# Kernel optimization log

Measured on AMD Instinct MI355X. Metric: run time of the kernel, lower is better.

The kernel has to match this reference:

```python
import jax, jax.numpy as jnp
import numpy as np

D_MODEL = 768
NUM_HEADS = 12
HEAD_DIM = D_MODEL // NUM_HEADS  # 64, also rotary dim
INTERMEDIATE = 1152
WINDOW = 128          # config.local_attention (layer_id=1 -> local layer)
ROPE_BASE = 10000.0   # local_rope_theta
EPS = 1e-5


def layer_norm_nocenter(x, gamma):
    # keras LayerNormalization(center=False): mean-subtract, no beta
    mu = jnp.mean(x, axis=-1, keepdims=True)
    var = jnp.var(x, axis=-1, keepdims=True)
    return (x - mu) * jax.lax.rsqrt(var + EPS) * gamma


def rotate_half(x):
    x1, x2 = jnp.split(x, 2, axis=-1)
    return jnp.concatenate([-x2, x1], axis=-1)


def setup_inputs() -> dict:
    key = jax.random.key(0)
    ks = jax.random.split(key, 7)
    B, S = 4, 2048
    hidden_states = jax.random.normal(ks[0], (B, S, D_MODEL), dtype=jnp.float32)
    attention_mask = jnp.zeros((B, 1, S, S), dtype=jnp.float32)  # no padding
    s = 0.02
    attn_norm_gamma = jnp.ones((D_MODEL,), dtype=jnp.float32)
    wqkv = jax.random.normal(ks[1], (D_MODEL, 3 * D_MODEL), dtype=jnp.float32) * s
    wo_attn = jax.random.normal(ks[2], (D_MODEL, D_MODEL), dtype=jnp.float32) * s
    mlp_norm_gamma = jnp.ones((D_MODEL,), dtype=jnp.float32)
    wi = jax.random.normal(ks[3], (D_MODEL, 2 * INTERMEDIATE), dtype=jnp.float32) * s
    wo_mlp = jax.random.normal(ks[4], (INTERMEDIATE, D_MODEL), dtype=jnp.float32) * s
    return {
        'hidden_states': hidden_states,
        'attention_mask': attention_mask,
        'attn_norm_gamma': attn_norm_gamma,
        'wqkv': wqkv,
        'wo_attn': wo_attn,
        'mlp_norm_gamma': mlp_norm_gamma,
        'wi': wi,
        'wo_mlp': wo_mlp,
    }


def reference(hidden_states, attention_mask, attn_norm_gamma, wqkv, wo_attn,
              mlp_norm_gamma, wi, wo_mlp):
    B, S, Dm = hidden_states.shape
    H, Dh = NUM_HEADS, HEAD_DIM

    # RoPE cache (NTKScaling with scaling_factor=1 -> plain RoPE)
    idx = jnp.arange(0, Dh, 2, dtype=jnp.float32)
    inv_freq = 1.0 / (ROPE_BASE ** (idx / Dh))          # [Dh/2]
    t = jnp.arange(S, dtype=jnp.float32)
    freqs = t[:, None] * inv_freq[None, :]              # [S, Dh/2]
    emb = jnp.concatenate([freqs, freqs], axis=-1)      # [S, Dh]
    cos = jnp.cos(emb)[None, None]                      # [1,1,S,Dh]
    sin = jnp.sin(emb)[None, None]

    # combined sliding-window + padding mask
    pos = jnp.arange(S)
    dist = jnp.abs(pos[:, None] - pos[None, :])
    neg = jnp.finfo(jnp.float32).min
    local = jnp.where(dist <= WINDOW // 2, 0.0, neg).astype(jnp.float32)
    mask = attention_mask + local[None, None]           # [B,1,S,S]

    # attention (layer_id != 0 -> pre-norm)
    x = layer_norm_nocenter(hidden_states, attn_norm_gamma)
    qkv = (x @ wqkv).reshape(B, S, 3, H, Dh).transpose(2, 0, 3, 1, 4)
    q, k, v = qkv[0], qkv[1], qkv[2]                    # [B,H,S,Dh]
    q = q * cos + rotate_half(q) * sin
    k = k * cos + rotate_half(k) * sin

    scale = 1.0 / jnp.sqrt(jnp.asarray(Dh, q.dtype))
    scores = jnp.einsum('bhqd,bhkd->bhqk', q, k) * scale + mask
    attn = jax.nn.softmax(scores, axis=-1)
    ctx = jnp.einsum('bhqk,bhkd->bhqd', attn, v)
    attn_out = ctx.transpose(0, 2, 1, 3).reshape(B, S, Dm) @ wo_attn

    h = hidden_states + attn_out

    # GLU MLP: Wi -> split -> gelu(x)*gate -> Wo, residual
    n = layer_norm_nocenter(h, mlp_norm_gamma)
    x_in, gate = jnp.split(n @ wi, 2, axis=-1)
    mlp = jax.nn.gelu(x_in, approximate=False) * gate
    return h + mlp @ wo_mlp
```

## Files before the change

kernel.cpp:

```cpp
#include <hip/hip_runtime.h>
#include <cstdint>
#include <cstddef>

typedef __bf16 bf16;
typedef float f32x4 __attribute__((ext_vector_type(4)));
typedef __bf16 bf16x8 __attribute__((ext_vector_type(8)));
typedef __bf16 bf16x4 __attribute__((ext_vector_type(4)));
typedef __bf16 bf16x2 __attribute__((ext_vector_type(2)));

#define MFMA16(a, b, c) __builtin_amdgcn_mfma_f32_16x16x32_bf16((a), (b), (c), 0, 0, 0)

__device__ __forceinline__ void gload_lds16(const void* g, void* l) {
  __builtin_amdgcn_global_load_lds((__attribute__((address_space(1))) void*)g,
                                   (__attribute__((address_space(3))) void*)l,
                                   16, 0, 0);
}

__global__ __launch_bounds__(256) void wconv_ln(const float* __restrict__ wqkv,
                                                const float* __restrict__ woa,
                                                const float* __restrict__ wi,
                                                const float* __restrict__ wom,
                                                bf16* __restrict__ wqkvT,
                                                bf16* __restrict__ woaT,
                                                bf16* __restrict__ wiT,
                                                bf16* __restrict__ womT,
                                                const float* __restrict__ X,
                                                const float* __restrict__ gamma,
                                                bf16* __restrict__ xnout) {
  __shared__ float tile[32][33];
  const int t = threadIdx.x;
  int id = blockIdx.x;
  if (id >= 4896) {
    const int row = id - 4896;
    const float* xr = X + (size_t)row * 768;
    float v0 = xr[t], v1 = xr[t + 256], v2 = xr[t + 512];
    float s = v0 + v1 + v2;
    float s2 = v0 * v0 + v1 * v1 + v2 * v2;
#pragma unroll
    for (int m = 1; m <= 32; m <<= 1) {
      s += __shfl_xor(s, m, 64);
      s2 += __shfl_xor(s2, m, 64);
    }
    float* red = &tile[0][0];
    const int w = t >> 6, lane = t & 63;
    if (lane == 0) { red[w] = s; red[4 + w] = s2; }
    __syncthreads();
    s = red[0] + red[1] + red[2] + red[3];
    s2 = red[4] + red[5] + red[6] + red[7];
    const float mu = s * (1.f / 768.f);
    const float var = s2 * (1.f / 768.f) - mu * mu;
    const float rs = rsqrtf(var + 1e-5f);
    xnout[(size_t)row * 768 + t] = (bf16)((v0 - mu) * rs * gamma[t]);
    xnout[(size_t)row * 768 + t + 256] = (bf16)((v1 - mu) * rs * gamma[t + 256]);
    xnout[(size_t)row * 768 + t + 512] = (bf16)((v2 - mu) * rs * gamma[t + 512]);
    return;
  }
  const float* W;
  bf16* Wt;
  int K, N, bx, by;
  if (id < 1728) { W = wqkv; Wt = wqkvT; K = 768; N = 2304; bx = id % 72; by = id / 72; }
  else if (id < 2304) { id -= 1728; W = woa; Wt = woaT; K = 768; N = 768; bx = id % 24; by = id / 24; }
  else if (id < 4032) { id -= 2304; W = wi; Wt = wiT; K = 768; N = 2304; bx = id % 72; by = id / 72; }
  else { id -= 4032; W = wom; Wt = womT; K = 1152; N = 768; bx = id % 24; by = id / 24; }
  const int n0 = bx * 32, k0 = by * 32;
  const int c = t & 31, r = t >> 5;
#pragma unroll
  for (int i = 0; i < 4; ++i)
    tile[r + i * 8][c] = W[(size_t)(k0 + r + i * 8) * N + n0 + c];
  __syncthreads();
#pragma unroll
  for (int i = 0; i < 4; ++i)
    Wt[(size_t)(n0 + r + i * 8) * K + k0 + c] = (bf16)tile[c][r + i * 8];
}

__global__ __launch_bounds__(256) void ln_kernel(const float* __restrict__ X,
                                                 const float* __restrict__ gamma,
                                                 bf16* __restrict__ out) {
  const int row = blockIdx.x, t = threadIdx.x;
  const float* xr = X + (size_t)row * 768;
  float v0 = xr[t], v1 = xr[t + 256], v2 = xr[t + 512];
  float s = v0 + v1 + v2;
  float s2 = v0 * v0 + v1 * v1 + v2 * v2;
#pragma unroll
  for (int m = 1; m <= 32; m <<= 1) {
    s += __shfl_xor(s, m, 64);
    s2 += __shfl_xor(s2, m, 64);
  }
  __shared__ float red[8];
  const int w = t >> 6, lane = t & 63;
  if (lane == 0) { red[w] = s; red[4 + w] = s2; }
  __syncthreads();
  s = red[0] + red[1] + red[2] + red[3];
  s2 = red[4] + red[5] + red[6] + red[7];
  const float mu = s * (1.f / 768.f);
  const float var = s2 * (1.f / 768.f) - mu * mu;
  const float rs = rsqrtf(var + 1e-5f);
  out[(size_t)row * 768 + t] = (bf16)((v0 - mu) * rs * gamma[t]);
  out[(size_t)row * 768 + t + 256] = (bf16)((v1 - mu) * rs * gamma[t + 256]);
  out[(size_t)row * 768 + t + 512] = (bf16)((v2 - mu) * rs * gamma[t + 512]);
}

#define GEMM_CORE_LOOP(NT_, AROW_EXPR, BROW_EXPR)                                   \
  auto stage = [&](int tile, int half) {                                            \
    const int kk0 = tile * 64;                                                      \
    bf16* Ab_ = &SM[(tile % 3) * 24576];                                            \
    bf16* Bb_ = Ab_ + 16384;                                                        \
    _Pragma("unroll") for (int i = 0; i < 2; ++i) {                                 \
      int c = (half * 2 + i) * 512 + t;                                             \
      int r = c >> 3, j = (c & 7) ^ (r & 7);                                        \
      gload_lds16(Ap + (size_t)(AROW_EXPR) * Kd + (kk0 + j * 8), &Ab_[c * 8]);      \
    }                                                                               \
    {                                                                               \
      int c = half * 512 + t;                                                       \
      int r = c >> 3, j = (c & 7) ^ (r & 7);                                        \
      gload_lds16(Bp + (size_t)(BROW_EXPR) * Kd + (kk0 + j * 8), &Bb_[c * 8]);      \
    }                                                                               \
  };                                                                                \
  stage(0, 0); stage(0, 1);                                                         \
  stage(1, 0); stage(1, 1);                                                         \
  asm volatile("s_waitcnt vmcnt(6)" ::: "memory");                                  \
  __builtin_amdgcn_s_barrier();                                                     \
  __builtin_amdgcn_sched_barrier(0);                                                \
  for (int tt = 0; tt < NT_; ++tt) {                                                \
    const bf16* Ab = &SM[(tt % 3) * 24576];                                         \
    const bf16* Bb = Ab + 16384;                                                    \
    bf16x8 af[4], bfr[4];                                                           \
                                                           \
    _Pragma("unroll") for (int mt = 0; mt < 4; ++mt) {                              \
      int r = wm * 64 + mt * 16 + rm;                                               \
      af[mt] = *(const bf16x8*)&Ab[r * 64 + ((qd ^ (r & 7)) * 8)];                  \
    }                                                                               \
    _Pragma("unroll") for (int nt = 0; nt < 4; ++nt) {                              \
      int r = wn * 64 + nt * 16 + rm;                                               \
      bfr[nt] = *(const bf16x8*)&Bb[r * 64 + ((qd ^ (r & 7)) * 8)];                 \
    }                                                                               \
    if (tt + 2 < NT_) stage(tt + 2, 0);                                             \
    __builtin_amdgcn_s_barrier();                                                   \
    __builtin_amdgcn_sched_barrier(0);                                              \
    asm volatile("s_waitcnt lgkmcnt(0)" ::: "memory");                              \
    __builtin_amdgcn_sched_barrier(0);                                              \
    __builtin_amdgcn_s_setprio(1);                                                  \
    _Pragma("unroll") for (int mt = 0; mt < 4; ++mt)                                \
      _Pragma("unroll") for (int nt = 0; nt < 4; ++nt)                              \
        acc[mt][nt] = MFMA16(af[mt], bfr[nt], acc[mt][nt]);                         \
    __builtin_amdgcn_s_setprio(0);                                                  \
    __builtin_amdgcn_s_barrier();                                                   \
    __builtin_amdgcn_sched_barrier(0);                                              \
                                                           \
    _Pragma("unroll") for (int mt = 0; mt < 4; ++mt) {                              \
      int r = wm * 64 + mt * 16 + rm;                                               \
      af[mt] = *(const bf16x8*)&Ab[r * 64 + (((4 + qd) ^ (r & 7)) * 8)];            \
    }                                                                               \
    _Pragma("unroll") for (int nt = 0; nt < 4; ++nt) {                              \
      int r = wn * 64 + nt * 16 + rm;                                               \
      bfr[nt] = *(const bf16x8*)&Bb[r * 64 + (((4 + qd) ^ (r & 7)) * 8)];           \
    }                                                                               \
    if (tt + 2 < NT_) stage(tt + 2, 1);                                             \
    __builtin_amdgcn_s_barrier();                                                   \
    __builtin_amdgcn_sched_barrier(0);                                              \
    asm volatile("s_waitcnt lgkmcnt(0)" ::: "memory");                              \
    __builtin_amdgcn_sched_barrier(0);                                              \
    __builtin_amdgcn_s_setprio(1);                                                  \
    _Pragma("unroll") for (int mt = 0; mt < 4; ++mt)                                \
      _Pragma("unroll") for (int nt = 0; nt < 4; ++nt)                              \
        acc[mt][nt] = MFMA16(af[mt], bfr[nt], acc[mt][nt]);                         \
    __builtin_amdgcn_s_setprio(0);                                                  \
    if (tt + 2 < NT_) { asm volatile("s_waitcnt vmcnt(6)" ::: "memory"); }          \
    else if (tt + 1 < NT_) { asm volatile("s_waitcnt vmcnt(0)" ::: "memory"); }     \
    __builtin_amdgcn_s_barrier();                                                   \
    __builtin_amdgcn_sched_barrier(0);                                              \
  }

template <int EPI, int NT>
__global__ __launch_bounds__(512, 2) void gemm_pipe(const bf16* __restrict__ Ap,
                                                    const bf16* __restrict__ Bp,
                                                    const float* __restrict__ Res,
                                                    void* __restrict__ Cout,
                                                    int Nout) {
  constexpr int Kd = NT * 64;
  __shared__ __align__(16) bf16 SM[73728];
  const int t = threadIdx.x;
  const int lane = t & 63, w = t >> 6;
  const int wm = w >> 1, wn = w & 1;
  const int rm = lane & 15, qd = lane >> 4;
  const int by = blockIdx.y;
  const int row0 = blockIdx.x * 256;
  f32x4 acc[4][4] = {};

  auto brow = [&](int r) -> int {
    if constexpr (EPI == 1) {
      int q = (r >> 4) & 3;
      return ((q & 1) ? 1152 : 0) + by * 64 + (r >> 6) * 32 + ((q >> 1) << 4) + (r & 15);
    } else {
      return by * 128 + r;
    }
  };

  GEMM_CORE_LOOP(NT, row0 + r, brow(r))

  if constexpr (EPI == 0) {
    float* C = (float*)Cout;
#pragma unroll
    for (int mt = 0; mt < 4; ++mt)
#pragma unroll
      for (int nt = 0; nt < 4; ++nt) {
        const int gc = by * 128 + wn * 64 + nt * 16 + rm;
#pragma unroll
        for (int r = 0; r < 4; ++r) {
          const int gr = row0 + wm * 64 + mt * 16 + qd * 4 + r;
          const size_t idx = (size_t)gr * Nout + gc;
          C[idx] = Res[idx] + acc[mt][nt][r];
        }
      }
  } else {
    bf16* C = (bf16*)Cout;
#pragma unroll
    for (int mt = 0; mt < 4; ++mt)
#pragma unroll
      for (int g = 0; g < 2; ++g) {
        const int gc = by * 64 + wn * 32 + g * 16 + rm;
#pragma unroll
        for (int r = 0; r < 4; ++r) {
          const int gr = row0 + wm * 64 + mt * 16 + qd * 4 + r;
          const float x = acc[mt][g * 2][r], gv = acc[mt][g * 2 + 1][r];
          const float ge = 0.5f * x * (1.0f + erff(x * 0.70710678118654752f));
          C[(size_t)gr * 1152 + gc] = (bf16)(ge * gv);
        }
      }
  }
}

__global__ __launch_bounds__(512, 2) void gemm_qkv3(const bf16* __restrict__ Ap,
                                                    const bf16* __restrict__ Bp,
                                                    bf16* __restrict__ Qb,
                                                    bf16* __restrict__ Kb,
                                                    bf16* __restrict__ Vt) {
  constexpr int Kd = 768;
  __shared__ __align__(16) bf16 SM[73728];
  const int t = threadIdx.x;
  const int lane = t & 63, w = t >> 6;
  const int wm = w >> 1, wn = w & 1;
  const int rm = lane & 15, qd = lane >> 4;
  const int by = blockIdx.y;
  const int row0 = blockIdx.x * 256;
  f32x4 acc[4][4] = {};

  GEMM_CORE_LOOP(12, row0 + r, by * 128 + r)

  const int head_id = by * 2 + wn;
  const int typ = by / 6;
  const int b = row0 >> 11;
  const int sblk = row0 & 2047;
  const int sw = sblk + wm * 64;

  if (typ < 2) {
    const int h = head_id - typ * 12;
    const size_t bhbase = (size_t)(b * 12 + h) * 2048;
    bf16* dst = typ ? Kb : Qb;
    constexpr float inv2pi = 0.15915494309189535f;
#pragma unroll
    for (int nt = 0; nt < 2; ++nt) {
      const int d = nt * 16 + rm;
      const float invf = exp2f((float)d * -0.41524101186092029f);
      float rev = (float)(sw + qd * 4) * invf * inv2pi;
      rev -= floorf(rev);
      float cs = __builtin_amdgcn_cosf(rev);
      float sn = __builtin_amdgcn_sinf(rev);
      float rv1 = invf * inv2pi;
      float c1 = __builtin_amdgcn_cosf(rv1), s1 = __builtin_amdgcn_sinf(rv1);
      float rv13 = 13.f * invf * inv2pi;
      rv13 -= floorf(rv13);
      float c13 = __builtin_amdgcn_cosf(rv13), s13 = __builtin_amdgcn_sinf(rv13);
#pragma unroll
      for (int mt = 0; mt < 4; ++mt)
#pragma unroll
        for (int r = 0; r < 4; ++r) {
          const int s = sw + mt * 16 + qd * 4 + r;
          const float x1 = acc[mt][nt][r], x2 = acc[mt][nt + 2][r];
          bf16x2 v2;
          v2[0] = (bf16)(x1 * cs - x2 * sn);
          v2[1] = (bf16)(x2 * cs + x1 * sn);
          *(bf16x2*)&dst[(bhbase + s) * 64 + 2 * d] = v2;
          const float ca = (r < 3) ? c1 : c13, sa = (r < 3) ? s1 : s13;
          const float cn = cs * ca - sn * sa;
          sn = sn * ca + cs * sa;
          cs = cn;
        }
    }
  } else {
#pragma unroll
    for (int mt = 0; mt < 4; ++mt)
#pragma unroll
      for (int nt = 0; nt < 4; ++nt) {
        int hd = wn * 64 + nt * 16 + rm;
        int sl = wm * 64 + mt * 16 + qd * 4;
        bf16x4 v4;
#pragma unroll
        for (int r = 0; r < 4; ++r) v4[r] = (bf16)acc[mt][nt][r];
        *(bf16x4*)&SM[hd * 264 + sl] = v4;
      }
    __syncthreads();
    const int h0 = by * 2 - 24;
#pragma unroll
    for (int it = 0; it < 8; ++it) {
      int cc = it * 512 + t;
      int hd = cc >> 5, s8 = (cc & 31) * 8;
      bf16x8 vv = *(const bf16x8*)&SM[hd * 264 + s8];
      size_t grow = (size_t)(b * 12 + h0 + (hd >> 6)) * 64 + (hd & 63);
      *(bf16x8*)&Vt[grow * 2048 + sblk + s8] = vv;
    }
  }
}

__global__ __launch_bounds__(256) void attn_kernel(const bf16* __restrict__ Qb,
                                                   const bf16* __restrict__ Kb,
                                                   const bf16* __restrict__ Vt,
                                                   const float* __restrict__ am,
                                                   bf16* __restrict__ ctx) {
  __shared__ __align__(16) bf16 KP[64 * 200];
  __shared__ __align__(16) bf16 Vts[64 * 192];
  bf16* Ks = KP;
  bf16* Ps = KP;

  const int t = threadIdx.x;
  const int lane = t & 63, w = t >> 6;
  const int rm = lane & 15, qd = lane >> 4;
  const int s0 = blockIdx.y * 64;
  const int bh = blockIdx.x;
  const int b = bh / 12, h = bh - b * 12;
  const size_t baseQ = (size_t)bh * 2048;

#pragma unroll
  for (int i = 0; i < 6; ++i) {
    int c = i * 256 + t;
    int r = c >> 3, j = (c & 7) ^ (r & 7);
    int key = min(max(s0 - 64 + r, 0), 2047);
    gload_lds16(Kb + (baseQ + key) * 64 + j * 8, &Ks[c * 8]);
  }
#pragma unroll
  for (int i = 0; i < 6; ++i) {
    int c = i * 256 + t;
    int r = c / 24, jl = c - r * 24;
    int j = (jl & 24) | ((jl & 7) ^ (r & 7));
    int k0 = min(max(s0 - 64 + j * 8, 0), 2040);
    gload_lds16(Vt + ((size_t)bh * 64 + r) * 2048 + k0, &Vts[c * 8]);
  }

  bf16x8 aq[2];
#pragma unroll
  for (int kb = 0; kb < 2; ++kb)
    aq[kb] = *(const bf16x8*)&Qb[(baseQ + s0 + w * 16 + rm) * 64 + kb * 32 + qd * 8];

  float msk[12][4];
#pragma unroll
  for (int nt = 0; nt < 12; ++nt) {
    int key = s0 - 64 + nt * 16 + rm;
#pragma unroll
    for (int r = 0; r < 4; ++r) {
      int qpos = s0 + w * 16 + qd * 4 + r;
      bool valid = (key >= 0) && (key < 2048) && (key - qpos <= 64) && (qpos - key <= 64);
      msk[nt][r] = valid ? am[((size_t)b * 2048 + qpos) * 2048 + key] : -3e38f;
    }
  }
  __syncthreads();

  f32x4 sc[12];
#pragma unroll
  for (int nt = 0; nt < 12; ++nt) {
    f32x4 a = {0.f, 0.f, 0.f, 0.f};
#pragma unroll
    for (int kb = 0; kb < 2; ++kb) {
      int r = nt * 16 + rm;
      bf16x8 bk = *(const bf16x8*)&Ks[r * 64 + (((kb * 4 + qd) ^ (rm & 7)) * 8)];
      a = MFMA16(aq[kb], bk, a);
    }
    sc[nt] = a;
  }

  float mx[4] = {-3e38f, -3e38f, -3e38f, -3e38f};
#pragma unroll
  for (int nt = 0; nt < 12; ++nt)
#pragma unroll
    for (int r = 0; r < 4; ++r) {
      float v = (msk[nt][r] <= -2.9e38f) ? -3e38f : sc[nt][r] * 0.125f + msk[nt][r];
      sc[nt][r] = v;
      mx[r] = fmaxf(mx[r], v);
    }
#pragma unroll
  for (int r = 0; r < 4; ++r)
#pragma unroll
    for (int m = 1; m <= 8; m <<= 1) mx[r] = fmaxf(mx[r], __shfl_xor(mx[r], m, 64));
  float sum[4] = {0.f, 0.f, 0.f, 0.f};
#pragma unroll
  for (int nt = 0; nt < 12; ++nt)
#pragma unroll
    for (int r = 0; r < 4; ++r) {
      float p = (sc[nt][r] > -1e37f) ? __expf(sc[nt][r] - mx[r]) : 0.f;
      sc[nt][r] = p;
      sum[r] += p;
    }
#pragma unroll
  for (int r = 0; r < 4; ++r)
#pragma unroll
    for (int m = 1; m <= 8; m <<= 1) sum[r] += __shfl_xor(sum[r], m, 64);
  float inv[4];
#pragma unroll
  for (int r = 0; r < 4; ++r) inv[r] = 1.f / sum[r];

  __syncthreads();

#pragma unroll
  for (int nt = 0; nt < 12; ++nt)
#pragma unroll
    for (int r = 0; r < 4; ++r)
      Ps[(w * 16 + qd * 4 + r) * 200 + nt * 16 + rm] = (bf16)(sc[nt][r] * inv[r]);

  f32x4 o[4] = {};
#pragma unroll
  for (int ks = 0; ks < 6; ++ks) {
    bf16x8 ap = *(const bf16x8*)&Ps[(w * 16 + rm) * 200 + ks * 32 + qd * 8];
#pragma unroll
    for (int nt = 0; nt < 4; ++nt) {
      int kc = ks * 4 + qd;
      bf16x8 bv = *(const bf16x8*)&Vts[(nt * 16 + rm) * 192 +
                                       (((kc & 24) | ((kc & 7) ^ (rm & 7))) * 8)];
      o[nt] = MFMA16(ap, bv, o[nt]);
    }
  }
#pragma unroll
  for (int nt = 0; nt < 4; ++nt)
#pragma unroll
    for (int r = 0; r < 4; ++r) {
      int q_ = s0 + w * 16 + qd * 4 + r;
      ctx[((size_t)(b * 2048 + q_)) * 768 + h * 64 + nt * 16 + rm] = (bf16)o[nt][r];
    }
}

extern "C" void kernel_launch(void* const* d_in, const int* in_sizes, int n_in,
                              void* d_out, int out_size, void* d_ws, size_t ws_size,
                              hipStream_t stream) {
  (void)in_sizes; (void)n_in; (void)out_size; (void)ws_size;
  const float* hidden = (const float*)d_in[0];
  const float* amask = (const float*)d_in[1];
  const float* g1 = (const float*)d_in[2];
  const float* wqkv = (const float*)d_in[3];
  const float* woa = (const float*)d_in[4];
  const float* g2 = (const float*)d_in[5];
  const float* wi = (const float*)d_in[6];
  const float* wom = (const float*)d_in[7];
  float* out = (float*)d_out;

  char* p = (char*)d_ws;
  size_t o = 0;
  auto take = [&](size_t bytes) {
    char* r = p + o;
    o = (o + bytes + 255) & ~(size_t)255;
    return r;
  };
  bf16* wqkvT = (bf16*)take((size_t)2304 * 768 * 2);
  bf16* woaT = (bf16*)take((size_t)768 * 768 * 2);
  bf16* wiT = (bf16*)take((size_t)2304 * 768 * 2);
  bf16* womT = (bf16*)take((size_t)768 * 1152 * 2);
  bf16* xn = (bf16*)take((size_t)8192 * 768 * 2);
  bf16* Qb = (bf16*)take((size_t)98304 * 64 * 2);
  bf16* Kb = (bf16*)take((size_t)98304 * 64 * 2);
  bf16* Vt = (bf16*)take((size_t)98304 * 64 * 2);
  bf16* ctxb = (bf16*)take((size_t)8192 * 768 * 2);
  float* hbuf = (float*)take((size_t)8192 * 768 * 4);
  bf16* mlp = (bf16*)take((size_t)8192 * 1152 * 2);

  wconv_ln<<<13088, 256, 0, stream>>>(wqkv, woa, wi, wom, wqkvT, woaT, wiT, womT,
                                      hidden, g1, xn);

  gemm_qkv3<<<dim3(32, 18), 512, 0, stream>>>(xn, wqkvT, Qb, Kb, Vt);
  attn_kernel<<<dim3(48, 32), 256, 0, stream>>>(Qb, Kb, Vt, amask, ctxb);
  gemm_pipe<0, 12><<<dim3(32, 6), 512, 0, stream>>>(ctxb, woaT, hidden, hbuf, 768);

  ln_kernel<<<8192, 256, 0, stream>>>(hbuf, g2, xn);
  gemm_pipe<1, 12><<<dim3(32, 18), 512, 0, stream>>>(xn, wiT, nullptr, mlp, 1152);
  gemm_pipe<0, 18><<<dim3(32, 6), 512, 0, stream>>>(mlp, womT, hbuf, out, 768);
}
```

Before: 292.0 us.

## Replace QKV and GLU GEMMs with single-buffered 128x256 tile kernels

The QKV projection and the GLU up-projection now use new 256-thread kernels in which each block computes a 128x256 output tile (four waves, each owning 128x64), instead of 512-thread 256x128 tiles with triple-buffered pipelining. The K-loop loads one 64-wide K slab per iteration into LDS and synchronizes twice, with no prefetch overlap. The aim is more MFMA work per wave, more register reuse of the B fragments and a better grid shape (64x9 blocks), at the cost of exposed global-load latency and higher register pressure from 128 accumulator registers per thread. The fused RoPE, V-transpose and GELU-gate epilogues are carried over to the new tiling.

New measurement: 318.1 us. +8.9%, slower.

```diff
diff --git a/kernel.cpp b/kernel.cpp
--- a/kernel.cpp
+++ b/kernel.cpp
@@ -100,6 +100,150 @@
   out[(size_t)row * 768 + t + 512] = (bf16)((v2 - mu) * rs * gamma[t + 512]);
 }
 
+#define FATCORE_KLOOP(KD_, AROW_EXPR, BROW_EXPR)                                    \
+  for (int k0 = 0; k0 < (KD_); k0 += 64) {                                          \
+    _Pragma("unroll") for (int i = 0; i < 4; ++i) {                                 \
+      int c = i * 256 + t;                                                          \
+      int r = c >> 3, j = (c & 7) ^ (r & 7);                                        \
+      gload_lds16(Ap + (size_t)(AROW_EXPR) * (KD_) + (k0 + j * 8), &As[c * 8]);     \
+    }                                                                               \
+    _Pragma("unroll") for (int i = 0; i < 8; ++i) {                                 \
+      int c = i * 256 + t;                                                          \
+      int r = c >> 3, j = (c & 7) ^ (r & 7);                                        \
+      gload_lds16(Bp + (size_t)(BROW_EXPR) * (KD_) + (k0 + j * 8), &Bs[c * 8]);     \
+    }                                                                               \
+    __syncthreads();                                                                \
+    _Pragma("unroll") for (int kb = 0; kb < 2; ++kb) {                              \
+      bf16x8 bfr[4];                                                                \
+      _Pragma("unroll") for (int nt = 0; nt < 4; ++nt) {                            \
+        int r = w * 64 + nt * 16 + rm;                                              \
+        bfr[nt] = *(const bf16x8*)&Bs[r * 64 + (((kb * 4 + qd) ^ (r & 7)) * 8)];    \
+      }                                                                             \
+      _Pragma("unroll") for (int mt = 0; mt < 8; ++mt) {                            \
+        int r = mt * 16 + rm;                                                       \
+        bf16x8 af = *(const bf16x8*)&As[r * 64 + (((kb * 4 + qd) ^ (r & 7)) * 8)];  \
+        _Pragma("unroll") for (int nt = 0; nt < 4; ++nt)                            \
+          acc[mt][nt] = MFMA16(af, bfr[nt], acc[mt][nt]);                           \
+      }                                                                             \
+    }                                                                               \
+    __syncthreads();                                                                \
+  }
+
+__global__ __launch_bounds__(256, 2) void gemm_qkv4(const bf16* __restrict__ Ap,
+                                                    const bf16* __restrict__ Bp,
+                                                    bf16* __restrict__ Qb,
+                                                    bf16* __restrict__ Kb,
+                                                    bf16* __restrict__ Vt) {
+  __shared__ __align__(16) bf16 SM[34048];
+  bf16* As = SM;
+  bf16* Bs = SM + 8192;
+  const int t = threadIdx.x;
+  const int lane = t & 63, w = t >> 6;
+  const int rm = lane & 15, qd = lane >> 4;
+  const int by = blockIdx.y;
+  const int row0 = blockIdx.x * 128;
+  f32x4 acc[8][4] = {};
+
+  FATCORE_KLOOP(768, row0 + r, by * 256 + r)
+
+  const int typ = by / 3;
+  const int b = row0 >> 11;
+  const int sblk = row0 & 2047;
+
+  if (typ < 2) {
+    const int h = (by % 3) * 4 + w;
+    const size_t bhbase = (size_t)(b * 12 + h) * 2048;
+    bf16* dst = typ ? Kb : Qb;
+    constexpr float inv2pi = 0.15915494309189535f;
+#pragma unroll
+    for (int nt = 0; nt < 2; ++nt) {
+      const int d = nt * 16 + rm;
+      const float invf = exp2f((float)d * -0.41524101186092029f);
+      float rev = (float)(sblk + qd * 4) * invf * inv2pi;
+      rev -= floorf(rev);
+      float cs = __builtin_amdgcn_cosf(rev);
+      float sn = __builtin_amdgcn_sinf(rev);
+      float rv1 = invf * inv2pi;
+      float c1 = __builtin_amdgcn_cosf(rv1), s1 = __builtin_amdgcn_sinf(rv1);
+      float rv13 = 13.f * invf * inv2pi;
+      rv13 -= floorf(rv13);
+      float c13 = __builtin_amdgcn_cosf(rv13), s13 = __builtin_amdgcn_sinf(rv13);
+#pragma unroll
+      for (int mt = 0; mt < 8; ++mt)
+#pragma unroll
+        for (int r = 0; r < 4; ++r) {
+          const int s = sblk + mt * 16 + qd * 4 + r;
+          const float x1 = acc[mt][nt][r], x2 = acc[mt][nt + 2][r];
+          bf16x2 v2;
+          v2[0] = (bf16)(x1 * cs - x2 * sn);
+          v2[1] = (bf16)(x2 * cs + x1 * sn);
+          *(bf16x2*)&dst[(bhbase + s) * 64 + 2 * d] = v2;
+          const float ca = (r < 3) ? c1 : c13, sa = (r < 3) ? s1 : s13;
+          const float cn = cs * ca - sn * sa;
+          sn = sn * ca + cs * sa;
+          cs = cn;
+        }
+    }
+  } else {
+#pragma unroll
+    for (int mt = 0; mt < 8; ++mt)
+#pragma unroll
+      for (int nt = 0; nt < 4; ++nt) {
+        int hd = w * 64 + nt * 16 + rm;
+        int sl = mt * 16 + qd * 4;
+        bf16x4 v4;
+#pragma unroll
+        for (int r = 0; r < 4; ++r) v4[r] = (bf16)acc[mt][nt][r];
+        *(bf16x4*)&SM[hd * 132 + sl] = v4;
+      }
+    __syncthreads();
+    const int h0 = (by - 6) * 4;
+#pragma unroll
+    for (int it = 0; it < 16; ++it) {
+      int cc = it * 256 + t;
+      int hd = cc >> 4, s8 = (cc & 15) * 8;
+      bf16x8 vv = *(const bf16x8*)&SM[hd * 132 + s8];
+      size_t grow = (size_t)(b * 12 + h0 + (hd >> 6)) * 64 + (hd & 63);
+      *(bf16x8*)&Vt[grow * 2048 + sblk + s8] = vv;
+    }
+  }
+}
+
+__global__ __launch_bounds__(256, 2) void gemm_glu(const bf16* __restrict__ Ap,
+                                                   const bf16* __restrict__ Bp,
+                                                   bf16* __restrict__ C) {
+  __shared__ __align__(16) bf16 SM[24576];
+  bf16* As = SM;
+  bf16* Bs = SM + 8192;
+  const int t = threadIdx.x;
+  const int lane = t & 63, w = t >> 6;
+  const int rm = lane & 15, qd = lane >> 4;
+  const int by = blockIdx.y;
+  const int row0 = blockIdx.x * 128;
+  f32x4 acc[8][4] = {};
+
+  auto brow = [&](int r) -> int {
+    int wn_ = r >> 6, nt_ = (r >> 4) & 3;
+    return ((nt_ & 1) ? 1152 : 0) + by * 128 + wn_ * 32 + ((nt_ >> 1) << 4) + (r & 15);
+  };
+
+  FATCORE_KLOOP(768, row0 + r, brow(r))
+
+#pragma unroll
+  for (int mt = 0; mt < 8; ++mt)
+#pragma unroll
+    for (int g = 0; g < 2; ++g) {
+      const int gc = by * 128 + w * 32 + g * 16 + rm;
+#pragma unroll
+      for (int r = 0; r < 4; ++r) {
+        const int gr = row0 + mt * 16 + qd * 4 + r;
+        const float x = acc[mt][g * 2][r], gv = acc[mt][g * 2 + 1][r];
+        const float ge = 0.5f * x * (1.0f + erff(x * 0.70710678118654752f));
+        C[(size_t)gr * 1152 + gc] = (bf16)(ge * gv);
+      }
+    }
+}
+
 #define GEMM_CORE_LOOP(NT_, AROW_EXPR, BROW_EXPR)                                   \
   auto stage = [&](int tile, int half) {                                            \
     const int kk0 = tile * 64;                                                      \
@@ -187,129 +331,23 @@
   const int row0 = blockIdx.x * 256;
   f32x4 acc[4][4] = {};
 
-  auto brow = [&](int r) -> int {
-    if constexpr (EPI == 1) {
-      int q = (r >> 4) & 3;
-      return ((q & 1) ? 1152 : 0) + by * 64 + (r >> 6) * 32 + ((q >> 1) << 4) + (r & 15);
-    } else {
-      return by * 128 + r;
-    }
-  };
+  auto brow = [&](int r) -> int { return by * 128 + r; };
 
   GEMM_CORE_LOOP(NT, row0 + r, brow(r))
 
-  if constexpr (EPI == 0) {
-    float* C = (float*)Cout;
-#pragma unroll
-    for (int mt = 0; mt < 4; ++mt)
-#pragma unroll
-      for (int nt = 0; nt < 4; ++nt) {
-        const int gc = by * 128 + wn * 64 + nt * 16 + rm;
-#pragma unroll
-        for (int r = 0; r < 4; ++r) {
-          const int gr = row0 + wm * 64 + mt * 16 + qd * 4 + r;
-          const size_t idx = (size_t)gr * Nout + gc;
-          C[idx] = Res[idx] + acc[mt][nt][r];
-        }
+  float* C = (float*)Cout;
+#pragma unroll
+  for (int mt = 0; mt < 4; ++mt)
+#pragma unroll
+    for (int nt = 0; nt < 4; ++nt) {
+      const int gc = by * 128 + wn * 64 + nt * 16 + rm;
+#pragma unroll
+      for (int r = 0; r < 4; ++r) {
+        const int gr = row0 + wm * 64 + mt * 16 + qd * 4 + r;
+        const size_t idx = (size_t)gr * Nout + gc;
+        C[idx] = Res[idx] + acc[mt][nt][r];
       }
-  } else {
-    bf16* C = (bf16*)Cout;
-#pragma unroll
-    for (int mt = 0; mt < 4; ++mt)
-#pragma unroll
-      for (int g = 0; g < 2; ++g) {
-        const int gc = by * 64 + wn * 32 + g * 16 + rm;
-#pragma unroll
-        for (int r = 0; r < 4; ++r) {
-          const int gr = row0 + wm * 64 + mt * 16 + qd * 4 + r;
-          const float x = acc[mt][g * 2][r], gv = acc[mt][g * 2 + 1][r];
-          const float ge = 0.5f * x * (1.0f + erff(x * 0.70710678118654752f));
-          C[(size_t)gr * 1152 + gc] = (bf16)(ge * gv);
-        }
-      }
-  }
-}
-
-__global__ __launch_bounds__(512, 2) void gemm_qkv3(const bf16* __restrict__ Ap,
-                                                    const bf16* __restrict__ Bp,
-                                                    bf16* __restrict__ Qb,
-                                                    bf16* __restrict__ Kb,
-                                                    bf16* __restrict__ Vt) {
-  constexpr int Kd = 768;
-  __shared__ __align__(16) bf16 SM[73728];
-  const int t = threadIdx.x;
-  const int lane = t & 63, w = t >> 6;
-  const int wm = w >> 1, wn = w & 1;
-  const int rm = lane & 15, qd = lane >> 4;
-  const int by = blockIdx.y;
-  const int row0 = blockIdx.x * 256;
-  f32x4 acc[4][4] = {};
-
-  GEMM_CORE_LOOP(12, row0 + r, by * 128 + r)
-
-  const int head_id = by * 2 + wn;
-  const int typ = by / 6;
-  const int b = row0 >> 11;
-  const int sblk = row0 & 2047;
-  const int sw = sblk + wm * 64;
-
-  if (typ < 2) {
-    const int h = head_id - typ * 12;
-    const size_t bhbase = (size_t)(b * 12 + h) * 2048;
-    bf16* dst = typ ? Kb : Qb;
-    constexpr float inv2pi = 0.15915494309189535f;
-#pragma unroll
-    for (int nt = 0; nt < 2; ++nt) {
-      const int d = nt * 16 + rm;
-      const float invf = exp2f((float)d * -0.41524101186092029f);
-      float rev = (float)(sw + qd * 4) * invf * inv2pi;
-      rev -= floorf(rev);
-      float cs = __builtin_amdgcn_cosf(rev);
-      float sn = __builtin_amdgcn_sinf(rev);
-      float rv1 = invf * inv2pi;
-      float c1 = __builtin_amdgcn_cosf(rv1), s1 = __builtin_amdgcn_sinf(rv1);
-      float rv13 = 13.f * invf * inv2pi;
-      rv13 -= floorf(rv13);
-      float c13 = __builtin_amdgcn_cosf(rv13), s13 = __builtin_amdgcn_sinf(rv13);
-#pragma unroll
-      for (int mt = 0; mt < 4; ++mt)
-#pragma unroll
-        for (int r = 0; r < 4; ++r) {
-          const int s = sw + mt * 16 + qd * 4 + r;
-          const float x1 = acc[mt][nt][r], x2 = acc[mt][nt + 2][r];
-          bf16x2 v2;
-          v2[0] = (bf16)(x1 * cs - x2 * sn);
-          v2[1] = (bf16)(x2 * cs + x1 * sn);
-          *(bf16x2*)&dst[(bhbase + s) * 64 + 2 * d] = v2;
-          const float ca = (r < 3) ? c1 : c13, sa = (r < 3) ? s1 : s13;
-          const float cn = cs * ca - sn * sa;
-          sn = sn * ca + cs * sa;
-          cs = cn;
-        }
-    }
-  } else {
-#pragma unroll
-    for (int mt = 0; mt < 4; ++mt)
-#pragma unroll
-      for (int nt = 0; nt < 4; ++nt) {
-        int hd = wn * 64 + nt * 16 + rm;
-        int sl = wm * 64 + mt * 16 + qd * 4;
-        bf16x4 v4;
-#pragma unroll
-        for (int r = 0; r < 4; ++r) v4[r] = (bf16)acc[mt][nt][r];
-        *(bf16x4*)&SM[hd * 264 + sl] = v4;
-      }
-    __syncthreads();
-    const int h0 = by * 2 - 24;
-#pragma unroll
-    for (int it = 0; it < 8; ++it) {
-      int cc = it * 512 + t;
-      int hd = cc >> 5, s8 = (cc & 31) * 8;
-      bf16x8 vv = *(const bf16x8*)&SM[hd * 264 + s8];
-      size_t grow = (size_t)(b * 12 + h0 + (hd >> 6)) * 64 + (hd & 63);
-      *(bf16x8*)&Vt[grow * 2048 + sblk + s8] = vv;
-    }
-  }
+    }
 }
 
 __global__ __launch_bounds__(256) void attn_kernel(const bf16* __restrict__ Qb,
@@ -472,11 +510,11 @@
   wconv_ln<<<13088, 256, 0, stream>>>(wqkv, woa, wi, wom, wqkvT, woaT, wiT, womT,
                                       hidden, g1, xn);
 
-  gemm_qkv3<<<dim3(32, 18), 512, 0, stream>>>(xn, wqkvT, Qb, Kb, Vt);
+  gemm_qkv4<<<dim3(64, 9), 256, 0, stream>>>(xn, wqkvT, Qb, Kb, Vt);
   attn_kernel<<<dim3(48, 32), 256, 0, stream>>>(Qb, Kb, Vt, amask, ctxb);
   gemm_pipe<0, 12><<<dim3(32, 6), 512, 0, stream>>>(ctxb, woaT, hidden, hbuf, 768);
 
   ln_kernel<<<8192, 256, 0, stream>>>(hbuf, g2, xn);
-  gemm_pipe<1, 12><<<dim3(32, 18), 512, 0, stream>>>(xn, wiT, nullptr, mlp, 1152);
+  gemm_glu<<<dim3(64, 9), 256, 0, stream>>>(xn, wiT, mlp);
   gemm_pipe<0, 18><<<dim3(32, 6), 512, 0, stream>>>(mlp, womT, hbuf, out, 768);
 }
```

## Use 256x256 tiles with double-buffered pipeline for QKV and GLU GEMMs

Applied to the files above, without the earlier changes.

The QKV projection and the GLU up-projection now run on a new 256x256 block tile with 8 waves in a 2x4 layout. Each wave computes 128x64, and the K-loop uses two LDS buffers with staging spread across four sub-steps. The larger tile doubles operand reuse per LDS load and halves the grid from 576 to 288 blocks. The cost is 128 accumulator registers per thread, 128 KB+ of LDS per block, which likely allows only one block per CU despite launch_bounds(512,2), and a shallower two-stage prefetch in place of the three-stage one.

After: 312.5 us. 7.0% more time.

```diff
diff --git a/kernel.cpp b/kernel.cpp
--- a/kernel.cpp
+++ b/kernel.cpp
@@ -100,6 +100,173 @@
   out[(size_t)row * 768 + t + 512] = (bf16)((v2 - mu) * rs * gamma[t + 512]);
 }
 
+#define GEMM8_CORE(NT_, AROW_EXPR, BROW_EXPR)                                       \
+  auto stageu = [&](int tile, int u) {                                              \
+    const int kk0 = tile * 64;                                                      \
+    bf16* buf = &SM[(tile & 1) * 32768];                                            \
+    int c = (u & 3) * 512 + t;                                                      \
+    int r = c >> 3, j = (c & 7) ^ (r & 7);                                          \
+    if (u < 4)                                                                      \
+      gload_lds16(Ap + (size_t)(AROW_EXPR) * Kd + (kk0 + j * 8), &buf[c * 8]);      \
+    else                                                                            \
+      gload_lds16(Bp + (size_t)(BROW_EXPR) * Kd + (kk0 + j * 8),                    \
+                  &buf[16384 + c * 8]);                                             \
+  };                                                                                \
+  _Pragma("unroll") for (int u = 0; u < 8; ++u) stageu(0, u);                       \
+  asm volatile("s_waitcnt vmcnt(0)" ::: "memory");                                  \
+  __builtin_amdgcn_s_barrier();                                                     \
+  __builtin_amdgcn_sched_barrier(0);                                                \
+  for (int tt = 0; tt < NT_; ++tt) {                                                \
+    const bf16* Ab = &SM[(tt & 1) * 32768];                                         \
+    const bf16* Bb = Ab + 16384;                                                    \
+    bf16x8 af[4], bfr[4];                                                           \
+    _Pragma("unroll") for (int q = 0; q < 4; ++q) {                                 \
+      const int kb = q >> 1, mh = q & 1;                                            \
+      if (mh == 0) {                                                                \
+        _Pragma("unroll") for (int nt = 0; nt < 4; ++nt) {                          \
+          int r = wn * 64 + nt * 16 + rm;                                           \
+          bfr[nt] = *(const bf16x8*)&Bb[r * 64 + (((kb * 4 + qd) ^ (r & 7)) * 8)];  \
+        }                                                                           \
+      }                                                                             \
+      _Pragma("unroll") for (int mt = 0; mt < 4; ++mt) {                            \
+        int r = wm * 128 + (mh * 4 + mt) * 16 + rm;                                 \
+        af[mt] = *(const bf16x8*)&Ab[r * 64 + (((kb * 4 + qd) ^ (r & 7)) * 8)];     \
+      }                                                                             \
+      if (tt + 1 < NT_) { stageu(tt + 1, 2 * q); stageu(tt + 1, 2 * q + 1); }       \
+      __builtin_amdgcn_s_barrier();                                                 \
+      __builtin_amdgcn_sched_barrier(0);                                            \
+      asm volatile("s_waitcnt lgkmcnt(0)" ::: "memory");                            \
+      __builtin_amdgcn_sched_barrier(0);                                            \
+      __builtin_amdgcn_s_setprio(1);                                                \
+      _Pragma("unroll") for (int mt = 0; mt < 4; ++mt)                              \
+        _Pragma("unroll") for (int nt = 0; nt < 4; ++nt)                            \
+          acc[mh * 4 + mt][nt] = MFMA16(af[mt], bfr[nt], acc[mh * 4 + mt][nt]);     \
+      __builtin_amdgcn_s_setprio(0);                                                \
+      if (q == 3 && tt + 1 < NT_) {                                                 \
+        asm volatile("s_waitcnt vmcnt(0)" ::: "memory");                            \
+      }                                                                             \
+      __builtin_amdgcn_s_barrier();                                                 \
+      __builtin_amdgcn_sched_barrier(0);                                            \
+    }                                                                               \
+  }
+
+__global__ __launch_bounds__(512, 2) void gemm_qkv8(const bf16* __restrict__ Ap,
+                                                    const bf16* __restrict__ Bp,
+                                                    bf16* __restrict__ Qb,
+                                                    bf16* __restrict__ Kb,
+                                                    bf16* __restrict__ Vt) {
+  constexpr int Kd = 768;
+  __shared__ __align__(16) bf16 SM[67584];
+  const int t = threadIdx.x;
+  const int lane = t & 63, w = t >> 6;
+  const int wm = w >> 2, wn = w & 3;
+  const int rm = lane & 15, qd = lane >> 4;
+  const int by = blockIdx.y;
+  const int row0 = blockIdx.x * 256;
+  f32x4 acc[8][4] = {};
+
+  GEMM8_CORE(12, row0 + r, by * 256 + r)
+
+  const int typ = by / 3;
+  const int b = row0 >> 11;
+  const int sblk = row0 & 2047;
+  const int sw = sblk + wm * 128;
+
+  if (typ < 2) {
+    const int h = (by % 3) * 4 + wn;
+    const size_t bhbase = (size_t)(b * 12 + h) * 2048;
+    bf16* dst = typ ? Kb : Qb;
+    constexpr float inv2pi = 0.15915494309189535f;
+#pragma unroll
+    for (int nt = 0; nt < 2; ++nt) {
+      const int d = nt * 16 + rm;
+      const float invf = exp2f((float)d * -0.41524101186092029f);
+      float rev = (float)(sw + qd * 4) * invf * inv2pi;
+      rev -= floorf(rev);
+      float cs = __builtin_amdgcn_cosf(rev);
+      float sn = __builtin_amdgcn_sinf(rev);
+      float rv1 = invf * inv2pi;
+      float c1 = __builtin_amdgcn_cosf(rv1), s1 = __builtin_amdgcn_sinf(rv1);
+      float rv13 = 13.f * invf * inv2pi;
+      rv13 -= floorf(rv13);
+      float c13 = __builtin_amdgcn_cosf(rv13), s13 = __builtin_amdgcn_sinf(rv13);
+#pragma unroll
+      for (int mt = 0; mt < 8; ++mt)
+#pragma unroll
+        for (int r = 0; r < 4; ++r) {
+          const int s = sw + mt * 16 + qd * 4 + r;
+          const float x1 = acc[mt][nt][r], x2 = acc[mt][nt + 2][r];
+          bf16x2 v2;
+          v2[0] = (bf16)(x1 * cs - x2 * sn);
+          v2[1] = (bf16)(x2 * cs + x1 * sn);
+          *(bf16x2*)&dst[(bhbase + s) * 64 + 2 * d] = v2;
+          const float ca = (r < 3) ? c1 : c13, sa = (r < 3) ? s1 : s13;
+          const float cn = cs * ca - sn * sa;
+          sn = sn * ca + cs * sa;
+          cs = cn;
+        }
+    }
+  } else {
+#pragma unroll
+    for (int mt = 0; mt < 8; ++mt)
+#pragma unroll
+      for (int nt = 0; nt < 4; ++nt) {
+        int hd = wn * 64 + nt * 16 + rm;
+        int sl = wm * 128 + mt * 16 + qd * 4;
+        bf16x4 v4;
+#pragma unroll
+        for (int r = 0; r < 4; ++r) v4[r] = (bf16)acc[mt][nt][r];
+        *(bf16x4*)&SM[hd * 264 + sl] = v4;
+      }
+    __syncthreads();
+    const int h0 = (by - 6) * 4;
+#pragma unroll
+    for (int it = 0; it < 16; ++it) {
+      int cc = it * 512 + t;
+      int hd = cc >> 5, s8 = (cc & 31) * 8;
+      bf16x8 vv = *(const bf16x8*)&SM[hd * 264 + s8];
+      size_t grow = (size_t)(b * 12 + h0 + (hd >> 6)) * 64 + (hd & 63);
+      *(bf16x8*)&Vt[grow * 2048 + sblk + s8] = vv;
+    }
+  }
+}
+
+__global__ __launch_bounds__(512, 2) void gemm_glu8(const bf16* __restrict__ Ap,
+                                                    const bf16* __restrict__ Bp,
+                                                    bf16* __restrict__ C) {
+  constexpr int Kd = 768;
+  __shared__ __align__(16) bf16 SM[65536];
+  const int t = threadIdx.x;
+  const int lane = t & 63, w = t >> 6;
+  const int wm = w >> 2, wn = w & 3;
+  const int rm = lane & 15, qd = lane >> 4;
+  const int by = blockIdx.y;
+  const int row0 = blockIdx.x * 256;
+  f32x4 acc[8][4] = {};
+
+  auto brow = [&](int r) -> int {
+    int q = (r >> 4) & 3;
+    return ((q & 1) ? 1152 : 0) + by * 128 + ((r >> 6) * 32) + (((q >> 1) & 1) * 16) +
+           (r & 15);
+  };
+
+  GEMM8_CORE(12, row0 + r, brow(r))
+
+#pragma unroll
+  for (int mt = 0; mt < 8; ++mt)
+#pragma unroll
+    for (int g = 0; g < 2; ++g) {
+      const int gc = by * 128 + wn * 32 + g * 16 + rm;
+#pragma unroll
+      for (int r = 0; r < 4; ++r) {
+        const int gr = row0 + wm * 128 + mt * 16 + qd * 4 + r;
+        const float x = acc[mt][g * 2][r], gv = acc[mt][g * 2 + 1][r];
+        const float ge = 0.5f * x * (1.0f + erff(x * 0.70710678118654752f));
+        C[(size_t)gr * 1152 + gc] = (bf16)(ge * gv);
+      }
+    }
+}
+
 #define GEMM_CORE_LOOP(NT_, AROW_EXPR, BROW_EXPR)                                   \
   auto stage = [&](int tile, int half) {                                            \
     const int kk0 = tile * 64;                                                      \
@@ -171,11 +338,11 @@
     __builtin_amdgcn_sched_barrier(0);                                              \
   }
 
-template <int EPI, int NT>
+template <int NT>
 __global__ __launch_bounds__(512, 2) void gemm_pipe(const bf16* __restrict__ Ap,
                                                     const bf16* __restrict__ Bp,
                                                     const float* __restrict__ Res,
-                                                    void* __restrict__ Cout,
+                                                    float* __restrict__ C,
                                                     int Nout) {
   constexpr int Kd = NT * 64;
   __shared__ __align__(16) bf16 SM[73728];
@@ -187,129 +354,20 @@
   const int row0 = blockIdx.x * 256;
   f32x4 acc[4][4] = {};
 
-  auto brow = [&](int r) -> int {
-    if constexpr (EPI == 1) {
-      int q = (r >> 4) & 3;
-      return ((q & 1) ? 1152 : 0) + by * 64 + (r >> 6) * 32 + ((q >> 1) << 4) + (r & 15);
-    } else {
-      return by * 128 + r;
-    }
-  };
-
-  GEMM_CORE_LOOP(NT, row0 + r, brow(r))
-
-  if constexpr (EPI == 0) {
-    float* C = (float*)Cout;
-#pragma unroll
-    for (int mt = 0; mt < 4; ++mt)
-#pragma unroll
-      for (int nt = 0; nt < 4; ++nt) {
-        const int gc = by * 128 + wn * 64 + nt * 16 + rm;
-#pragma unroll
-        for (int r = 0; r < 4; ++r) {
-          const int gr = row0 + wm * 64 + mt * 16 + qd * 4 + r;
-          const size_t idx = (size_t)gr * Nout + gc;
-          C[idx] = Res[idx] + acc[mt][nt][r];
-        }
+  GEMM_CORE_LOOP(NT, row0 + r, by * 128 + r)
+
+#pragma unroll
+  for (int mt = 0; mt < 4; ++mt)
+#pragma unroll
+    for (int nt = 0; nt < 4; ++nt) {
+      const int gc = by * 128 + wn * 64 + nt * 16 + rm;
+#pragma unroll
+      for (int r = 0; r < 4; ++r) {
+        const int gr = row0 + wm * 64 + mt * 16 + qd * 4 + r;
+        const size_t idx = (size_t)gr * Nout + gc;
+        C[idx] = Res[idx] + acc[mt][nt][r];
       }
-  } else {
-    bf16* C = (bf16*)Cout;
-#pragma unroll
-    for (int mt = 0; mt < 4; ++mt)
-#pragma unroll
-      for (int g = 0; g < 2; ++g) {
-        const int gc = by * 64 + wn * 32 + g * 16 + rm;
-#pragma unroll
-        for (int r = 0; r < 4; ++r) {
-          const int gr = row0 + wm * 64 + mt * 16 + qd * 4 + r;
-          const float x = acc[mt][g * 2][r], gv = acc[mt][g * 2 + 1][r];
-          const float ge = 0.5f * x * (1.0f + erff(x * 0.70710678118654752f));
-          C[(size_t)gr * 1152 + gc] = (bf16)(ge * gv);
-        }
-      }
-  }
-}
-
-__global__ __launch_bounds__(512, 2) void gemm_qkv3(const bf16* __restrict__ Ap,
-                                                    const bf16* __restrict__ Bp,
-                                                    bf16* __restrict__ Qb,
-                                                    bf16* __restrict__ Kb,
-                                                    bf16* __restrict__ Vt) {
-  constexpr int Kd = 768;
-  __shared__ __align__(16) bf16 SM[73728];
-  const int t = threadIdx.x;
-  const int lane = t & 63, w = t >> 6;
-  const int wm = w >> 1, wn = w & 1;
-  const int rm = lane & 15, qd = lane >> 4;
-  const int by = blockIdx.y;
-  const int row0 = blockIdx.x * 256;
-  f32x4 acc[4][4] = {};
-
-  GEMM_CORE_LOOP(12, row0 + r, by * 128 + r)
-
-  const int head_id = by * 2 + wn;
-  const int typ = by / 6;
-  const int b = row0 >> 11;
-  const int sblk = row0 & 2047;
-  const int sw = sblk + wm * 64;
-
-  if (typ < 2) {
-    const int h = head_id - typ * 12;
-    const size_t bhbase = (size_t)(b * 12 + h) * 2048;
-    bf16* dst = typ ? Kb : Qb;
-    constexpr float inv2pi = 0.15915494309189535f;
-#pragma unroll
-    for (int nt = 0; nt < 2; ++nt) {
-      const int d = nt * 16 + rm;
-      const float invf = exp2f((float)d * -0.41524101186092029f);
-      float rev = (float)(sw + qd * 4) * invf * inv2pi;
-      rev -= floorf(rev);
-      float cs = __builtin_amdgcn_cosf(rev);
-      float sn = __builtin_amdgcn_sinf(rev);
-      float rv1 = invf * inv2pi;
-      float c1 = __builtin_amdgcn_cosf(rv1), s1 = __builtin_amdgcn_sinf(rv1);
-      float rv13 = 13.f * invf * inv2pi;
-      rv13 -= floorf(rv13);
-      float c13 = __builtin_amdgcn_cosf(rv13), s13 = __builtin_amdgcn_sinf(rv13);
-#pragma unroll
-      for (int mt = 0; mt < 4; ++mt)
-#pragma unroll
-        for (int r = 0; r < 4; ++r) {
-          const int s = sw + mt * 16 + qd * 4 + r;
-          const float x1 = acc[mt][nt][r], x2 = acc[mt][nt + 2][r];
-          bf16x2 v2;
-          v2[0] = (bf16)(x1 * cs - x2 * sn);
-          v2[1] = (bf16)(x2 * cs + x1 * sn);
-          *(bf16x2*)&dst[(bhbase + s) * 64 + 2 * d] = v2;
-          const float ca = (r < 3) ? c1 : c13, sa = (r < 3) ? s1 : s13;
-          const float cn = cs * ca - sn * sa;
-          sn = sn * ca + cs * sa;
-          cs = cn;
-        }
-    }
-  } else {
-#pragma unroll
-    for (int mt = 0; mt < 4; ++mt)
-#pragma unroll
-      for (int nt = 0; nt < 4; ++nt) {
-        int hd = wn * 64 + nt * 16 + rm;
-        int sl = wm * 64 + mt * 16 + qd * 4;
-        bf16x4 v4;
-#pragma unroll
-        for (int r = 0; r < 4; ++r) v4[r] = (bf16)acc[mt][nt][r];
-        *(bf16x4*)&SM[hd * 264 + sl] = v4;
-      }
-    __syncthreads();
-    const int h0 = by * 2 - 24;
-#pragma unroll
-    for (int it = 0; it < 8; ++it) {
-      int cc = it * 512 + t;
-      int hd = cc >> 5, s8 = (cc & 31) * 8;
-      bf16x8 vv = *(const bf16x8*)&SM[hd * 264 + s8];
-      size_t grow = (size_t)(b * 12 + h0 + (hd >> 6)) * 64 + (hd & 63);
-      *(bf16x8*)&Vt[grow * 2048 + sblk + s8] = vv;
-    }
-  }
+    }
 }
 
 __global__ __launch_bounds__(256) void attn_kernel(const bf16* __restrict__ Qb,
@@ -472,11 +530,11 @@
   wconv_ln<<<13088, 256, 0, stream>>>(wqkv, woa, wi, wom, wqkvT, woaT, wiT, womT,
                                       hidden, g1, xn);
 
-  gemm_qkv3<<<dim3(32, 18), 512, 0, stream>>>(xn, wqkvT, Qb, Kb, Vt);
+  gemm_qkv8<<<dim3(32, 9), 512, 0, stream>>>(xn, wqkvT, Qb, Kb, Vt);
   attn_kernel<<<dim3(48, 32), 256, 0, stream>>>(Qb, Kb, Vt, amask, ctxb);
-  gemm_pipe<0, 12><<<dim3(32, 6), 512, 0, stream>>>(ctxb, woaT, hidden, hbuf, 768);
+  gemm_pipe<12><<<dim3(32, 6), 512, 0, stream>>>(ctxb, woaT, hidden, hbuf, 768);
 
   ln_kernel<<<8192, 256, 0, stream>>>(hbuf, g2, xn);
-  gemm_pipe<1, 12><<<dim3(32, 18), 512, 0, stream>>>(xn, wiT, nullptr, mlp, 1152);
-  gemm_pipe<0, 18><<<dim3(32, 6), 512, 0, stream>>>(mlp, womT, hbuf, out, 768);
-}
+  gemm_glu8<<<dim3(32, 9), 512, 0, stream>>>(xn, wiT, mlp);
+  gemm_pipe<18><<<dim3(32, 6), 512, 0, stream>>>(mlp, womT, hbuf, out, 768);
+}
```
